# Kernel optimization log

Hardware: AMD Instinct MI355X
Metric: run time of the kernel (lower is better)

The kernel has to match this reference:

```python
import jax, jax.numpy as jnp
import numpy as np

B, C, H, W = 256, 512, 14, 14
HW = H * W
TAU = 0.03          # args.tau
EPS = 0.65          # args.epsilon
EPS2 = 0.40         # args.epsilon - args.epsilon_margin
T_LOGIT = 0.07      # args.logit_temperature
MAX_ITERS = 32      # static unrolled bound for the data-dependent while-loop
PD_EPS = 1e-6       # torch.nn.PairwiseDistance default eps (added to the difference)


def setup_inputs() -> dict:
    key = jax.random.key(0)
    k1, k2 = jax.random.split(key)
    img = jax.random.normal(k1, (B, C, H, W), jnp.float32)
    img = img / (jnp.linalg.norm(img, axis=1, keepdims=True) + 1e-12)  # L2 over channels
    aud = jax.random.normal(k2, (B, C), jnp.float32)
    aud = aud / (jnp.linalg.norm(aud, axis=1, keepdims=True) + 1e-12)
    return {"img": img, "aud": aud}


def reference(img, aud):
    Bb, Cc, Hh, Ww = img.shape
    n_pix = Hh * Ww

    # PosLogits: [B,1,H,W]; Alllogits: [B,B,H,W]
    pos_logits = jnp.einsum('ncqa,nc->nqa', img, aud)[:, None]
    all_logits = jnp.einsum('ncqa,kc->nkqa', img, aud)

    # trimap negatives
    pos2 = jax.nn.sigmoid((pos_logits - EPS2) / TAU)
    neg = 1.0 - pos2                                        # [B,1,H,W]

    logit = img.reshape(Bb, Cc, -1) * pos_logits.reshape(Bb, 1, -1)   # [B,C,HW]
    positive0 = pos_logits.reshape(Bb, -1)                            # [B,HW]
    neg_val = (logit * neg.reshape(Bb, 1, -1)).mean(axis=2)           # [B,C]

    logit_t = logit.transpose(0, 2, 1)                                 # [B,HW,C]
    dist_to_zero = jnp.linalg.norm(logit_t - neg_val[:, None, :] + PD_EPS, axis=-1)  # [B,HW]

    def body(t, state):
        positive, already_pos, endpoint, obj = state
        idx = jnp.argmax(positive, axis=1)                             # [B] (detached in torch)
        sel = jnp.take_along_axis(logit, idx[:, None, None], axis=2)[:, :, 0]  # [B,C]
        obj = obj.at[t].set(sel * (~endpoint)[:, None].astype(sel.dtype))
        dist_to_logit = jnp.linalg.norm(logit_t - sel[:, None, :] + PD_EPS, axis=-1)  # [B,HW]
        pos = (dist_to_logit < dist_to_zero) & (~already_pos)
        already_pos = already_pos | pos
        positive = positive * (1.0 - pos.astype(positive.dtype))
        endpoint = endpoint | (pos.sum(axis=1) == 0) | (positive.max(axis=1) < 0.1)
        return (positive, already_pos, endpoint, obj)

    obj0 = jnp.zeros((MAX_ITERS, Bb, Cc), img.dtype)
    state0 = (positive0,
              jnp.zeros((Bb, n_pix), bool),
              jnp.zeros((Bb,), bool),
              obj0)
    _, _, _, object_arr = jax.lax.fori_loop(0, MAX_ITERS, body, state0)

    # lvs contrastive loss
    mask = 1.0 - 100.0 * jnp.eye(Bb, dtype=img.dtype)
    pos_m = jax.nn.sigmoid((pos_logits - EPS) / TAU)                   # [B,1,H,W]
    pos_all = jax.nn.sigmoid((all_logits - EPS) / TAU)                 # [B,B,H,W]
    sim1 = (pos_m * pos_logits).reshape(Bb, 1, -1).sum(-1) / pos_m.reshape(Bb, 1, -1).sum(-1)
    sim = (pos_all * all_logits).reshape(Bb, Bb, -1).sum(-1) / pos_all.reshape(Bb, Bb, -1).sum(-1) * mask
    sim2 = (neg * pos_logits).reshape(Bb, 1, -1).sum(-1) / neg.reshape(Bb, 1, -1).sum(-1)
    logits = jnp.concatenate((sim1, sim, sim2), axis=1) / T_LOGIT      # [B, B+2]
    loss = -jax.nn.log_softmax(logits, axis=1)[:, 0].mean()           # CE with target 0

    return loss, pos_logits[:, 0], object_arr
```

## Files before the change

### kernel.cpp

```cpp
#include <hip/hip_runtime.h>
#include <hip/hip_bf16.h>
#include <math.h>

#define NB 256
#define NC 512
#define NP 196
#define NIT 32
#define PROWS 208
#define LSTR 72
#define SFSTR 211

typedef __attribute__((ext_vector_type(8))) short bf16x8;
typedef __attribute__((ext_vector_type(4))) float f32x4;

__device__ __forceinline__ float sigf(float z){ return 1.0f/(1.0f+expf(-z)); }

__device__ __forceinline__ unsigned short f2bf(float x){
  return __bfloat16_as_ushort(__float2bfloat16(x));
}
__device__ __forceinline__ float bf2f(unsigned short h){
  union{float f; unsigned u;} v; v.u = ((unsigned)h)<<16; return v.f;
}
__device__ __forceinline__ double dshfl_xor(double v, int m){
  int lo = __shfl_xor(__double2loint(v), m);
  int hi = __shfl_xor(__double2hiint(v), m);
  return __hiloint2double(hi, lo);
}

__global__ __launch_bounds__(256) void aud2bf_kernel(const float* __restrict__ aud, unsigned short* __restrict__ aud_bf)
{
  int i = blockIdx.x*256 + threadIdx.x;
  aud_bf[i] = f2bf(aud[i]);
}


__global__ __launch_bounds__(512) void convert4_kernel(
    const float* __restrict__ img, const float* __restrict__ aud,
    unsigned short* __restrict__ hiT, unsigned short* __restrict__ loT,
    double* __restrict__ ppl, double* __restrict__ pcs)
{
  const int bid = blockIdx.x;
  const int b = bid & 255, part = bid >> 8;
  const int tid = threadIdx.x;
  const float* imgb = img + (size_t)b*NC*NP + (size_t)part*64*NP;
  __shared__ float sf[64*SFSTR];
  __shared__ float s_aud[64];
  if (tid < 64) s_aud[tid] = aud[b*NC + part*64 + tid];

  for (int j=tid; j<64*49; j+=512){
    int p4 = j % 49, c = j / 49;
    float4 v = *(const float4*)&imgb[(size_t)c*NP + p4*4];
    sf[c*SFSTR + p4*4+0]=v.x; sf[c*SFSTR + p4*4+1]=v.y;
    sf[c*SFSTR + p4*4+2]=v.z; sf[c*SFSTR + p4*4+3]=v.w;
  }
  __syncthreads();

  unsigned short* hp = hiT + (size_t)(b*8+part)*PROWS*64;
  unsigned short* lp = loT + (size_t)(b*8+part)*PROWS*64;
  for (int j=tid; j<PROWS*8; j+=512){
    int p = j>>3, o = j&7;
    unsigned hw[4], lw[4];
    double dot=0.0, sm=0.0;
    #pragma unroll
    for (int k2=0;k2<4;++k2){
      int c = o*8 + 2*k2;
      float x0 = (p<NP) ? sf[c*SFSTR + p]     : 0.f;
      float x1 = (p<NP) ? sf[(c+1)*SFSTR + p] : 0.f;
      unsigned short h0=f2bf(x0), h1=f2bf(x1);
      unsigned short l0=f2bf(x0-bf2f(h0)), l1=f2bf(x1-bf2f(h1));
      hw[k2] = (unsigned)h0 | ((unsigned)h1<<16);
      lw[k2] = (unsigned)l0 | ((unsigned)l1<<16);
      dot += (double)x0*(double)s_aud[c] + (double)x1*(double)s_aud[c+1];
      sm  += (double)x0 + (double)x1;
    }
    if (p < NP){
      *(uint4*)&hp[p*64 + o*8] = *(uint4*)hw;
      *(uint4*)&lp[p*64 + o*8] = *(uint4*)lw;
    }
    dot += dshfl_xor(dot,1); dot += dshfl_xor(dot,2); dot += dshfl_xor(dot,4);
    sm  += dshfl_xor(sm,1);  sm  += dshfl_xor(sm,2);  sm  += dshfl_xor(sm,4);
    if (o==0 && p<NP){
      ppl[(size_t)(b*8+part)*NP + p] = dot;
      pcs[(size_t)(b*8+part)*NP + p] = sm;
    }
  }
}

__global__ __launch_bounds__(256) void prep3_kernel(
    const double* __restrict__ ppl, const double* __restrict__ pcs,
    float* __restrict__ pl, float* __restrict__ cs,
    float* __restrict__ sim1, float* __restrict__ sim2, float* __restrict__ out_pl)
{
  const int b = blockIdx.x, tid = threadIdx.x;
  __shared__ double s_redd[256];
  float plv=0.f;
  if (tid < NP){
    double a=0.0, s=0.0;
    #pragma unroll
    for (int part=0; part<8; ++part){
      a += ppl[(size_t)(b*8+part)*NP + tid];
      s += pcs[(size_t)(b*8+part)*NP + tid];
    }
    plv=(float)a;
    float csv=(float)s;
    pl[b*NP+tid]=plv; cs[b*NP+tid]=csv; out_pl[b*NP+tid]=plv;
  }
  float pmw = (tid<NP)? sigf((plv-0.65f)/0.03f) : 0.f;
  float negw= (tid<NP)? 1.0f - sigf((plv-0.40f)/0.03f) : 0.f;
  double r[4];
  r[0]=(tid<NP)?(double)pmw*(double)plv:0.0;
  r[1]=(tid<NP)?(double)pmw:0.0;
  r[2]=(tid<NP)?(double)negw*(double)plv:0.0;
  r[3]=(tid<NP)?(double)negw:0.0;
  double res[4];
  for (int i=0;i<4;++i){
    __syncthreads();
    s_redd[tid]=r[i];
    __syncthreads();
    for (int s=128;s>0;s>>=1){ if (tid<s) s_redd[tid]+=s_redd[tid+s]; __syncthreads(); }
    res[i]=s_redd[0];
  }
  if (tid==0){
    sim1[b]=(float)(res[0]/res[1]);
    sim2[b]=(float)(res[2]/res[3]);
  }
}

__global__ __launch_bounds__(512) void gram2_kernel(
    const unsigned short* __restrict__ hiT, const unsigned short* __restrict__ loT,
    float* __restrict__ G)
{
  const int bid = blockIdx.x;
  const int b = bid & 255, h = bid >> 8;
  const int cbase = 7*h, ncl = 7 - h;
  const int tid = threadIdx.x, lane = tid & 63, w = tid >> 6;
  const int nr = (w<5)?2:1;
  const unsigned short* hb = hiT + (size_t)b*8*PROWS*64;
  const unsigned short* lb = loT + (size_t)b*8*PROWS*64;
  float* Gb = G + (size_t)b*NP*NP;
  __shared__ short smh[PROWS*LSTR];
  __shared__ short sml[PROWS*LSTR];

  f32x4 acc[2][7];
  #pragma unroll
  for (int i=0;i<2;++i)
    #pragma unroll
    for (int j=0;j<7;++j) acc[i][j]=(f32x4){0,0,0,0};

  for (int sl=0; sl<8; ++sl){
    __syncthreads();
    for (int j=tid; j<PROWS*8; j+=512){
      int p = j>>3, o = j&7;
      size_t src = ((size_t)sl*PROWS + p)*64 + o*8;
      *(uint4*)&smh[p*LSTR + o*8] = *(const uint4*)(hb + src);
      *(uint4*)&sml[p*LSTR + o*8] = *(const uint4*)(lb + src);
    }
    __syncthreads();
    #pragma unroll
    for (int kk=0; kk<2; ++kk){
      bf16x8 Ah[2], Al[2];
      #pragma unroll
      for (int i=0;i<2;++i){
        if (i<nr){
          int r = (w + 8*i)*16 + (lane&15);
          Ah[i] = *(const bf16x8*)&smh[r*LSTR + kk*32 + (lane>>4)*8];
          Al[i] = *(const bf16x8*)&sml[r*LSTR + kk*32 + (lane>>4)*8];
        }
      }
      #pragma unroll
      for (int j=0;j<7;++j){
        if (j<ncl){
          int r = (cbase+j)*16 + (lane&15);
          bf16x8 Bh = *(const bf16x8*)&smh[r*LSTR + kk*32 + (lane>>4)*8];
          bf16x8 Bl = *(const bf16x8*)&sml[r*LSTR + kk*32 + (lane>>4)*8];
          #pragma unroll
          for (int i=0;i<2;++i){
            if (i<nr){
              acc[i][j] = __builtin_amdgcn_mfma_f32_16x16x32_bf16(Ah[i], Bh, acc[i][j], 0,0,0);
              acc[i][j] = __builtin_amdgcn_mfma_f32_16x16x32_bf16(Ah[i], Bl, acc[i][j], 0,0,0);
              acc[i][j] = __builtin_amdgcn_mfma_f32_16x16x32_bf16(Al[i], Bh, acc[i][j], 0,0,0);
            }
          }
        }
      }
    }
  }

  const int r0 = (lane>>4)*4, colL = lane & 15;
  #pragma unroll
  for (int i=0;i<2;++i){
    #pragma unroll
    for (int j=0;j<7;++j){
      if (i<nr && j<ncl){
        int row = (w+8*i)*16 + r0;
        int col = (cbase+j)*16 + colL;
        if (col < NP){
          #pragma unroll
          for (int jj=0;jj<4;++jj){
            if (row+jj < NP) Gb[(size_t)(row+jj)*NP + col] = acc[i][j][jj];
          }
        }
      }
    }
  }
}

__global__ __launch_bounds__(512) void simgemm2_kernel(
    const unsigned short* __restrict__ hiT, const unsigned short* __restrict__ aud_bf,
    float* __restrict__ sumWA, float* __restrict__ sumW)
{
  const int bid = blockIdx.x;
  const int b = bid & 255, h = bid >> 8;
  const int tid = threadIdx.x, lane = tid & 63, w = tid >> 6;
  const int wr = w >> 2, wc = w & 3;
  const int pbase = (wr==0)?0:7, npt = 7-wr;
  const unsigned short* hb = hiT + (size_t)b*8*PROWS*64;
  __shared__ short smh[PROWS*LSTR];
  __shared__ short sma[128*LSTR];
  __shared__ float sred[2][2][4][2][16];

  f32x4 acc[7][2];
  #pragma unroll
  for (int i=0;i<7;++i)
    #pragma unroll
    for (int n=0;n<2;++n) acc[i][n]=(f32x4){0,0,0,0};

  for (int sl=0; sl<8; ++sl){
    __syncthreads();
    for (int j=tid; j<PROWS*8; j+=512){
      int p = j>>3, o = j&7;
      *(uint4*)&smh[p*LSTR + o*8] = *(const uint4*)(hb + ((size_t)sl*PROWS + p)*64 + o*8);
    }
    for (int j=tid; j<128*8; j+=512){
      int n = j>>3, o = j&7;
      *(uint4*)&sma[n*LSTR + o*8] = *(const uint4*)(aud_bf + (size_t)(h*128+n)*NC + sl*64 + o*8);
    }
    __syncthreads();
    #pragma unroll
    for (int kk=0; kk<2; ++kk){
      bf16x8 Ah[7];
      #pragma unroll
      for (int i=0;i<7;++i){
        if (i<npt){
          int r = (pbase+i)*16 + (lane&15);
          Ah[i] = *(const bf16x8*)&smh[r*LSTR + kk*32 + (lane>>4)*8];
        }
      }
      #pragma unroll
      for (int n=0;n<2;++n){
        int r = (wc*2+n)*16 + (lane&15);
        bf16x8 Bn = *(const bf16x8*)&sma[r*LSTR + kk*32 + (lane>>4)*8];
        #pragma unroll
        for (int i=0;i<7;++i)
          if (i<npt)
            acc[i][n] = __builtin_amdgcn_mfma_f32_16x16x32_bf16(Ah[i], Bn, acc[i][n], 0,0,0);
      }
    }
  }

  float swa[2]={0,0}, sw[2]={0,0};
  #pragma unroll
  for (int n=0;n<2;++n){
    #pragma unroll
    for (int i=0;i<7;++i){
      if (i<npt){
        int rowbase = (pbase+i)*16 + (lane>>4)*4;
        #pragma unroll
        for (int jj=0;jj<4;++jj){
          if (rowbase+jj < NP){
            float v = acc[i][n][jj];
            float wgt = sigf((v-0.65f)/0.03f);
            swa[n] += wgt*v; sw[n] += wgt;
          }
        }
      }
    }
  }
  #pragma unroll
  for (int n=0;n<2;++n){
    swa[n] += __shfl_xor(swa[n],16); swa[n] += __shfl_xor(swa[n],32);
    sw[n]  += __shfl_xor(sw[n],16);  sw[n]  += __shfl_xor(sw[n],32);
  }
  if (lane < 16){
    #pragma unroll
    for (int n=0;n<2;++n){
      sred[0][wr][wc][n][lane] = swa[n];
      sred[1][wr][wc][n][lane] = sw[n];
    }
  }
  __syncthreads();
  if (tid < 128){
    int wc2 = tid>>5, n2 = (tid>>4)&1, col = tid&15;
    float a = sred[0][0][wc2][n2][col] + sred[0][1][wc2][n2][col];
    float s = sred[1][0][wc2][n2][col] + sred[1][1][wc2][n2][col];
    int kcol = h*128 + (wc2*2+n2)*16 + col;
    sumWA[(size_t)b*NB + kcol] = a;
    sumW [(size_t)b*NB + kcol] = s;
  }
}

__global__ __launch_bounds__(1024) void loop4_kernel(
    const float* __restrict__ pl, const float* __restrict__ cs,
    const float* __restrict__ G, int* __restrict__ qseq, int* __restrict__ zf)
{
  const int b = blockIdx.x, tid = threadIdx.x, lane = tid & 63, w = tid >> 6;
  const float* Gb = G + (size_t)b*NP*NP;
  __shared__ float sG[NP*NP];
  __shared__ float s_pl[NP], s_wl[NP], s_csL[NP], s_gd[NP];
  __shared__ double gwd[NP];
  __shared__ double s_wred[16];
  __shared__ double s_bc;

  #pragma unroll
  for (int k=0;k<10;++k){
    int j = k*1024 + tid;
    if (j < NP*NP/4) ((float4*)sG)[j] = ((const float4*)Gb)[j];
  }
  float negw_t = 0.f;
  if (tid < NP){
    float plv = pl[b*NP+tid];
    float csv = cs[b*NP+tid];
    s_pl[tid] = plv;
    s_csL[tid] = plv*csv;
    negw_t = 1.0f - sigf((plv-0.40f)/0.03f);
    s_wl[tid] = plv*negw_t;
    s_gd[tid] = Gb[(size_t)tid*NP + tid];
  }
  __syncthreads();

  {
    int p = tid >> 2, qg = tid & 3;
    double a = 0.0;
    if (p < NP){
      for (int q=qg*49; q<qg*49+49; ++q) a += (double)sG[q*NP + p] * (double)s_wl[q];
    }
    a += dshfl_xor(a,1); a += dshfl_xor(a,2);
    if (qg==0 && p<NP) gwd[p] = a;
  }
  __syncthreads();

  double r = (tid<NP) ? (double)s_wl[tid]*gwd[tid] : 0.0;
  #pragma unroll
  for (int m=1;m<64;m<<=1) r += dshfl_xor(r,m);
  if (lane==0) s_wred[w] = r;
  __syncthreads();
  if (tid==0){ double t=0.0; for (int i=0;i<16;++i) t += s_wred[i]; s_bc = t; }
  __syncthreads();
  const double S2 = s_bc;
  __syncthreads();

  r = (tid<NP) ? (double)negw_t*(double)s_csL[tid] : 0.0;
  #pragma unroll
  for (int m=1;m<64;m<<=1) r += dshfl_xor(r,m);
  if (lane==0) s_wred[w] = r;
  __syncthreads();
  if (tid==0){ double t=0.0; for (int i=0;i<16;++i) t += s_wred[i]; s_bc = t; }
  __syncthreads();
  const double Swl = s_bc;
  __syncthreads();

  if (tid < NP){
    const double e = (double)1e-6f;
    double pld = (double)s_pl[tid];
    double d0sq = pld*pld*(double)s_gd[tid]
                - (2.0/196.0)*pld*gwd[tid]
                + S2/(196.0*196.0)
                + 2.0*e*((double)s_csL[tid] - Swl/196.0)
                + 512.0*e*e;
    if (d0sq < 0.0) d0sq = 0.0;
    gwd[tid] = d0sq;
  }
  __syncthreads();

  if (w != 0) return;

  float plv[4], csL[4], gdd[4], posv[4];
  double d0sq[4];
  bool alr[4];
  #pragma unroll
  for (int s=0;s<4;++s){
    int p = lane + 64*s;
    bool valid = p < NP;
    plv[s]  = valid ? s_pl[p]  : 0.f;
    csL[s]  = valid ? s_csL[p] : 0.f;
    gdd[s]  = valid ? s_gd[p]  : 0.f;
    d0sq[s] = valid ? gwd[p]   : 0.0;
    posv[s] = valid ? plv[s]   : -INFINITY;
    alr[s] = false;
  }
  bool endp = false;

  for (int t=0;t<NIT;++t){
    float v = posv[0]; int ix = lane;
    #pragma unroll
    for (int s=1;s<4;++s){
      if (posv[s] > v){ v = posv[s]; ix = lane + 64*s; }
    }
    #pragma unroll
    for (int m=1;m<64;m<<=1){
      float vv = __shfl_xor(v, m);
      int   ii = __shfl_xor(ix, m);
      if (vv>v || (vv==v && ii<ix)){ v=vv; ix=ii; }
    }
    const int q = ix;
    const float plq  = s_pl[q];
    const float gqq  = s_gd[q];
    const float csLq = s_csL[q];
    if (lane==0){ qseq[b*NIT+t] = q; zf[b*NIT+t] = endp ? 1 : 0; }

    int cnt = 0;
    #pragma unroll
    for (int s=0;s<4;++s){
      int p = lane + 64*s;
      if (p<NP && !alr[s]){
        float Gpq = sG[q*NP + p];
        double plp=(double)plv[s], dq=(double)plq;
        const double e=(double)1e-6f;
        double d2 = plp*plp*(double)gdd[s]
                  - 2.0*plp*dq*(double)Gpq
                  + dq*dq*(double)gqq
                  + 2.0*e*((double)csL[s]-(double)csLq)
                  + 512.0*e*e;
        if (d2<0.0) d2=0.0;
        if (d2 < d0sq[s]){ alr[s]=true; posv[s]=posv[s]*0.0f; cnt++; }
      }
    }
    float mx = fmaxf(fmaxf(posv[0],posv[1]),fmaxf(posv[2],posv[3]));
    #pragma unroll
    for (int m=1;m<64;m<<=1){
      cnt += __shfl_xor(cnt, m);
      mx = fmaxf(mx, __shfl_xor(mx, m));
    }
    if (cnt==0 || mx<0.1f) endp=true;
  }
}

__global__ __launch_bounds__(64) void objw_kernel(
    const unsigned short* __restrict__ hiT, const unsigned short* __restrict__ loT,
    const float* __restrict__ pl, const int* __restrict__ qseq, const int* __restrict__ zf,
    float* __restrict__ obj)
{
  const int bid = blockIdx.x;
  const int b = bid >> 5, t = bid & 31;
  const int lane = threadIdx.x;
  float* op = obj + ((size_t)t*NB + b)*NC;
  const int z = zf[b*NIT + t];
  if (z){
    float4 zv = {0.f,0.f,0.f,0.f};
    *(float4*)&op[lane*8]   = zv;
    *(float4*)&op[lane*8+4] = zv;
    return;
  }
  const int q = qseq[b*NIT + t];
  const float plq = pl[b*NP + q];
  const int part = lane >> 3, off = lane & 7;
  size_t src = ((size_t)(b*8+part)*PROWS + q)*64 + off*8;
  uint4 hv = *(const uint4*)(hiT + src);
  uint4 lv = *(const uint4*)(loT + src);
  const unsigned* hw = (const unsigned*)&hv;
  const unsigned* lw = (const unsigned*)&lv;
  float o8[8];
  #pragma unroll
  for (int k2=0;k2<4;++k2){
    float x0 = bf2f((unsigned short)(hw[k2]&0xffff)) + bf2f((unsigned short)(lw[k2]&0xffff));
    float x1 = bf2f((unsigned short)(hw[k2]>>16))    + bf2f((unsigned short)(lw[k2]>>16));
    o8[2*k2]   = x0*plq;
    o8[2*k2+1] = x1*plq;
  }
  *(float4*)&op[lane*8]   = *(float4*)&o8[0];
  *(float4*)&op[lane*8+4] = *(float4*)&o8[4];
}

__global__ __launch_bounds__(256) void finalize_b(
    const float* __restrict__ sim1, const float* __restrict__ sim2,
    const float* __restrict__ sumWA, const float* __restrict__ sumW,
    float* __restrict__ lossb)
{
  const int b = blockIdx.x, k = threadIdx.x;
  __shared__ float s_red[256];
  __shared__ double s_redd[256];
  const float T = 0.07f;
  float s = sumWA[(size_t)b*NB+k]/sumW[(size_t)b*NB+k];
  if (k==b) s *= -99.0f;
  const float lk = s/T;
  const float l0 = sim1[b]/T, ll = sim2[b]/T;
  s_red[k]=lk; __syncthreads();
  for (int st=128;st>0;st>>=1){ if(k<st) s_red[k]=fmaxf(s_red[k],s_red[k+st]); __syncthreads(); }
  const float m = fmaxf(s_red[0], fmaxf(l0,ll));
  __syncthreads();
  double e = (double)expf(lk-m);
  if (k==0) e += (double)expf(l0-m)+(double)expf(ll-m);
  s_redd[k]=e; __syncthreads();
  for (int st=128;st>0;st>>=1){ if(k<st) s_redd[k]+=s_redd[k+st]; __syncthreads(); }
  if (k==0) lossb[b] = -(float)((double)(l0-m) - log(s_redd[0]));
}

__global__ __launch_bounds__(256) void finalize_sum(const float* __restrict__ lossb, float* __restrict__ out_loss)
{
  const int tid = threadIdx.x;
  __shared__ double sr[256];
  sr[tid]=(double)lossb[tid]; __syncthreads();
  for (int st=128;st>0;st>>=1){ if(tid<st) sr[tid]+=sr[tid+st]; __syncthreads(); }
  if (tid==0) out_loss[0]=(float)(sr[0]/256.0);
}

extern "C" void kernel_launch(void* const* d_in, const int* in_sizes, int n_in,
                              void* d_out, int out_size, void* d_ws, size_t ws_size,
                              hipStream_t stream)
{
  const float* img = (const float*)d_in[0];
  const float* aud = (const float*)d_in[1];
  float* out = (float*)d_out;
  float* ws  = (float*)d_ws;

  float* pl    = ws;
  float* cs    = pl    + NB*NP;
  float* sim1  = cs    + NB*NP;
  float* sim2  = sim1  + NB;
  float* sumWA = sim2  + NB;
  float* sumW  = sumWA + NB*NB;
  unsigned short* aud_bf = (unsigned short*)(sumW + NB*NB);
  float* G     = (float*)(aud_bf + NB*NC);
  unsigned short* hiT = (unsigned short*)(G + (size_t)NB*NP*NP);
  unsigned short* loT = hiT + (size_t)NB*8*PROWS*64;
  int* qseq    = (int*)(loT + (size_t)NB*8*PROWS*64);
  int* zf      = qseq + NB*NIT;
  float* lossb = (float*)(zf + NB*NIT);

  double* ppl = (double*)G;
  double* pcs = ppl + (size_t)NB*8*NP;

  float* out_loss = out;
  float* out_pl   = out + 1;
  float* out_obj  = out + 1 + NB*NP;

  hipLaunchKernelGGL(aud2bf_kernel,   dim3(NB*NC/256), dim3(256),  0, stream, aud, aud_bf);
  hipLaunchKernelGGL(convert4_kernel, dim3(NB*8),      dim3(512),  0, stream, img, aud, hiT, loT, ppl, pcs);
  hipLaunchKernelGGL(prep3_kernel,    dim3(NB),        dim3(256),  0, stream, ppl, pcs, pl, cs, sim1, sim2, out_pl);
  hipLaunchKernelGGL(gram2_kernel,    dim3(NB*2),      dim3(512),  0, stream, hiT, loT, G);
  hipLaunchKernelGGL(loop4_kernel,    dim3(NB),        dim3(1024), 0, stream, pl, cs, G, qseq, zf);
  hipLaunchKernelGGL(simgemm2_kernel, dim3(NB*2),      dim3(512),  0, stream, hiT, aud_bf, sumWA, sumW);
  hipLaunchKernelGGL(objw_kernel,     dim3(NB*NIT),    dim3(64),   0, stream, hiT, loT, pl, qseq, zf, out_obj);
  hipLaunchKernelGGL(finalize_b,      dim3(NB),        dim3(256),  0, stream, sim1, sim2, sumWA, sumW, lossb);
  hipLaunchKernelGGL(finalize_sum,    dim3(1),         dim3(256),  0, stream, lossb, out_loss);
}
```

Measured before the change: 200.2 us.

## Fuse gram and sim GEMMs, fold aud conversion and obj writeback into neighbours

```diff
diff --git a/kernel.cpp b/kernel.cpp
--- a/kernel.cpp
+++ b/kernel.cpp
@@ -27,16 +27,11 @@
   return __hiloint2double(hi, lo);
 }
 
-__global__ __launch_bounds__(256) void aud2bf_kernel(const float* __restrict__ aud, unsigned short* __restrict__ aud_bf)
-{
-  int i = blockIdx.x*256 + threadIdx.x;
-  aud_bf[i] = f2bf(aud[i]);
-}
-
 
 __global__ __launch_bounds__(512) void convert4_kernel(
     const float* __restrict__ img, const float* __restrict__ aud,
     unsigned short* __restrict__ hiT, unsigned short* __restrict__ loT,
+    unsigned short* __restrict__ aud_bf,
     double* __restrict__ ppl, double* __restrict__ pcs)
 {
   const int bid = blockIdx.x;
@@ -45,6 +40,7 @@
   const float* imgb = img + (size_t)b*NC*NP + (size_t)part*64*NP;
   __shared__ float sf[64*SFSTR];
   __shared__ float s_aud[64];
+  if (part == 0) aud_bf[b*NC + tid] = f2bf(aud[b*NC + tid]);
   if (tid < 64) s_aud[tid] = aud[b*NC + part*64 + tid];
 
   for (int j=tid; j<64*49; j+=512){
@@ -126,182 +122,180 @@
   }
 }
 
-__global__ __launch_bounds__(512) void gram2_kernel(
+__global__ __launch_bounds__(512) void gramsim_kernel(
     const unsigned short* __restrict__ hiT, const unsigned short* __restrict__ loT,
-    float* __restrict__ G)
+    const unsigned short* __restrict__ aud_bf,
+    float* __restrict__ G, float* __restrict__ sumWA, float* __restrict__ sumW)
 {
   const int bid = blockIdx.x;
-  const int b = bid & 255, h = bid >> 8;
-  const int cbase = 7*h, ncl = 7 - h;
+  const int xcd = bid & 7, k = bid >> 3;
+  const int b = xcd + 8*(k>>2), role = k & 3;
   const int tid = threadIdx.x, lane = tid & 63, w = tid >> 6;
-  const int nr = (w<5)?2:1;
   const unsigned short* hb = hiT + (size_t)b*8*PROWS*64;
   const unsigned short* lb = loT + (size_t)b*8*PROWS*64;
-  float* Gb = G + (size_t)b*NP*NP;
-  __shared__ short smh[PROWS*LSTR];
-  __shared__ short sml[PROWS*LSTR];
-
-  f32x4 acc[2][7];
-  #pragma unroll
-  for (int i=0;i<2;++i)
-    #pragma unroll
-    for (int j=0;j<7;++j) acc[i][j]=(f32x4){0,0,0,0};
-
-  for (int sl=0; sl<8; ++sl){
-    __syncthreads();
-    for (int j=tid; j<PROWS*8; j+=512){
-      int p = j>>3, o = j&7;
-      size_t src = ((size_t)sl*PROWS + p)*64 + o*8;
-      *(uint4*)&smh[p*LSTR + o*8] = *(const uint4*)(hb + src);
-      *(uint4*)&sml[p*LSTR + o*8] = *(const uint4*)(lb + src);
-    }
-    __syncthreads();
-    #pragma unroll
-    for (int kk=0; kk<2; ++kk){
-      bf16x8 Ah[2], Al[2];
-      #pragma unroll
-      for (int i=0;i<2;++i){
-        if (i<nr){
-          int r = (w + 8*i)*16 + (lane&15);
-          Ah[i] = *(const bf16x8*)&smh[r*LSTR + kk*32 + (lane>>4)*8];
-          Al[i] = *(const bf16x8*)&sml[r*LSTR + kk*32 + (lane>>4)*8];
-        }
-      }
-      #pragma unroll
-      for (int j=0;j<7;++j){
-        if (j<ncl){
-          int r = (cbase+j)*16 + (lane&15);
-          bf16x8 Bh = *(const bf16x8*)&smh[r*LSTR + kk*32 + (lane>>4)*8];
-          bf16x8 Bl = *(const bf16x8*)&sml[r*LSTR + kk*32 + (lane>>4)*8];
-          #pragma unroll
-          for (int i=0;i<2;++i){
-            if (i<nr){
-              acc[i][j] = __builtin_amdgcn_mfma_f32_16x16x32_bf16(Ah[i], Bh, acc[i][j], 0,0,0);
-              acc[i][j] = __builtin_amdgcn_mfma_f32_16x16x32_bf16(Ah[i], Bl, acc[i][j], 0,0,0);
-              acc[i][j] = __builtin_amdgcn_mfma_f32_16x16x32_bf16(Al[i], Bh, acc[i][j], 0,0,0);
+  __shared__ short smA[PROWS*LSTR];
+  __shared__ short smB[PROWS*LSTR];
+  __shared__ float sred[2][2][4][2][16];
+
+  if (role < 2){
+    const int h = role;
+    const int cbase = 7*h, ncl = 7 - h;
+    const int nr = (w<5)?2:1;
+    float* Gb = G + (size_t)b*NP*NP;
+
+    f32x4 acc[2][7];
+    #pragma unroll
+    for (int i=0;i<2;++i)
+      #pragma unroll
+      for (int j=0;j<7;++j) acc[i][j]=(f32x4){0,0,0,0};
+
+    for (int sl=0; sl<8; ++sl){
+      __syncthreads();
+      for (int j=tid; j<PROWS*8; j+=512){
+        int p = j>>3, o = j&7;
+        size_t src = ((size_t)sl*PROWS + p)*64 + o*8;
+        *(uint4*)&smA[p*LSTR + o*8] = *(const uint4*)(hb + src);
+        *(uint4*)&smB[p*LSTR + o*8] = *(const uint4*)(lb + src);
+      }
+      __syncthreads();
+      #pragma unroll
+      for (int kk=0; kk<2; ++kk){
+        bf16x8 Ah[2], Al[2];
+        #pragma unroll
+        for (int i=0;i<2;++i){
+          if (i<nr){
+            int r = (w + 8*i)*16 + (lane&15);
+            Ah[i] = *(const bf16x8*)&smA[r*LSTR + kk*32 + (lane>>4)*8];
+            Al[i] = *(const bf16x8*)&smB[r*LSTR + kk*32 + (lane>>4)*8];
+          }
+        }
+        #pragma unroll
+        for (int j=0;j<7;++j){
+          if (j<ncl){
+            int r = (cbase+j)*16 + (lane&15);
+            bf16x8 Bh = *(const bf16x8*)&smA[r*LSTR + kk*32 + (lane>>4)*8];
+            bf16x8 Bl = *(const bf16x8*)&smB[r*LSTR + kk*32 + (lane>>4)*8];
+            #pragma unroll
+            for (int i=0;i<2;++i){
+              if (i<nr){
+                acc[i][j] = __builtin_amdgcn_mfma_f32_16x16x32_bf16(Ah[i], Bh, acc[i][j], 0,0,0);
+                acc[i][j] = __builtin_amdgcn_mfma_f32_16x16x32_bf16(Ah[i], Bl, acc[i][j], 0,0,0);
+                acc[i][j] = __builtin_amdgcn_mfma_f32_16x16x32_bf16(Al[i], Bh, acc[i][j], 0,0,0);
+              }
             }
           }
         }
       }
     }
-  }
-
-  const int r0 = (lane>>4)*4, colL = lane & 15;
-  #pragma unroll
-  for (int i=0;i<2;++i){
-    #pragma unroll
-    for (int j=0;j<7;++j){
-      if (i<nr && j<ncl){
-        int row = (w+8*i)*16 + r0;
-        int col = (cbase+j)*16 + colL;
-        if (col < NP){
+
+    const int r0 = (lane>>4)*4, colL = lane & 15;
+    #pragma unroll
+    for (int i=0;i<2;++i){
+      #pragma unroll
+      for (int j=0;j<7;++j){
+        if (i<nr && j<ncl){
+          int row = (w+8*i)*16 + r0;
+          int col = (cbase+j)*16 + colL;
+          if (col < NP){
+            #pragma unroll
+            for (int jj=0;jj<4;++jj){
+              if (row+jj < NP) Gb[(size_t)(row+jj)*NP + col] = acc[i][j][jj];
+            }
+          }
+        }
+      }
+    }
+  } else {
+    const int h = role - 2;
+    const int wr = w >> 2, wc = w & 3;
+    const int pbase = (wr==0)?0:7, npt = 7-wr;
+
+    f32x4 acc[7][2];
+    #pragma unroll
+    for (int i=0;i<7;++i)
+      #pragma unroll
+      for (int n=0;n<2;++n) acc[i][n]=(f32x4){0,0,0,0};
+
+    for (int sl=0; sl<8; ++sl){
+      __syncthreads();
+      for (int j=tid; j<PROWS*8; j+=512){
+        int p = j>>3, o = j&7;
+        *(uint4*)&smA[p*LSTR + o*8] = *(const uint4*)(hb + ((size_t)sl*PROWS + p)*64 + o*8);
+      }
+      for (int j=tid; j<128*8; j+=512){
+        int n = j>>3, o = j&7;
+        *(uint4*)&smB[n*LSTR + o*8] = *(const uint4*)(aud_bf + (size_t)(h*128+n)*NC + sl*64 + o*8);
+      }
+      __syncthreads();
+      #pragma unroll
+      for (int kk=0; kk<2; ++kk){
+        bf16x8 Ah[7];
+        #pragma unroll
+        for (int i=0;i<7;++i){
+          if (i<npt){
+            int r = (pbase+i)*16 + (lane&15);
+            Ah[i] = *(const bf16x8*)&smA[r*LSTR + kk*32 + (lane>>4)*8];
+          }
+        }
+        #pragma unroll
+        for (int n=0;n<2;++n){
+          int r = (wc*2+n)*16 + (lane&15);
+          bf16x8 Bn = *(const bf16x8*)&smB[r*LSTR + kk*32 + (lane>>4)*8];
+          #pragma unroll
+          for (int i=0;i<7;++i)
+            if (i<npt)
+              acc[i][n] = __builtin_amdgcn_mfma_f32_16x16x32_bf16(Ah[i], Bn, acc[i][n], 0,0,0);
+        }
+      }
+    }
+
+    float swa[2]={0,0}, sw[2]={0,0};
+    #pragma unroll
+    for (int n=0;n<2;++n){
+      #pragma unroll
+      for (int i=0;i<7;++i){
+        if (i<npt){
+          int rowbase = (pbase+i)*16 + (lane>>4)*4;
           #pragma unroll
           for (int jj=0;jj<4;++jj){
-            if (row+jj < NP) Gb[(size_t)(row+jj)*NP + col] = acc[i][j][jj];
+            if (rowbase+jj < NP){
+              float v = acc[i][n][jj];
+              float wgt = sigf((v-0.65f)/0.03f);
+              swa[n] += wgt*v; sw[n] += wgt;
+            }
           }
         }
       }
     }
-  }
-}
-
-__global__ __launch_bounds__(512) void simgemm2_kernel(
-    const unsigned short* __restrict__ hiT, const unsigned short* __restrict__ aud_bf,
-    float* __restrict__ sumWA, float* __restrict__ sumW)
-{
-  const int bid = blockIdx.x;
-  const int b = bid & 255, h = bid >> 8;
-  const int tid = threadIdx.x, lane = tid & 63, w = tid >> 6;
-  const int wr = w >> 2, wc = w & 3;
-  const int pbase = (wr==0)?0:7, npt = 7-wr;
-  const unsigned short* hb = hiT + (size_t)b*8*PROWS*64;
-  __shared__ short smh[PROWS*LSTR];
-  __shared__ short sma[128*LSTR];
-  __shared__ float sred[2][2][4][2][16];
-
-  f32x4 acc[7][2];
-  #pragma unroll
-  for (int i=0;i<7;++i)
-    #pragma unroll
-    for (int n=0;n<2;++n) acc[i][n]=(f32x4){0,0,0,0};
-
-  for (int sl=0; sl<8; ++sl){
+    #pragma unroll
+    for (int n=0;n<2;++n){
+      swa[n] += __shfl_xor(swa[n],16); swa[n] += __shfl_xor(swa[n],32);
+      sw[n]  += __shfl_xor(sw[n],16);  sw[n]  += __shfl_xor(sw[n],32);
+    }
+    if (lane < 16){
+      #pragma unroll
+      for (int n=0;n<2;++n){
+        sred[0][wr][wc][n][lane] = swa[n];
+        sred[1][wr][wc][n][lane] = sw[n];
+      }
+    }
     __syncthreads();
-    for (int j=tid; j<PROWS*8; j+=512){
-      int p = j>>3, o = j&7;
-      *(uint4*)&smh[p*LSTR + o*8] = *(const uint4*)(hb + ((size_t)sl*PROWS + p)*64 + o*8);
-    }
-    for (int j=tid; j<128*8; j+=512){
-      int n = j>>3, o = j&7;
-      *(uint4*)&sma[n*LSTR + o*8] = *(const uint4*)(aud_bf + (size_t)(h*128+n)*NC + sl*64 + o*8);
-    }
-    __syncthreads();
-    #pragma unroll
-    for (int kk=0; kk<2; ++kk){
-      bf16x8 Ah[7];
-      #pragma unroll
-      for (int i=0;i<7;++i){
-        if (i<npt){
-          int r = (pbase+i)*16 + (lane&15);
-          Ah[i] = *(const bf16x8*)&smh[r*LSTR + kk*32 + (lane>>4)*8];
-        }
-      }
-      #pragma unroll
-      for (int n=0;n<2;++n){
-        int r = (wc*2+n)*16 + (lane&15);
-        bf16x8 Bn = *(const bf16x8*)&sma[r*LSTR + kk*32 + (lane>>4)*8];
-        #pragma unroll
-        for (int i=0;i<7;++i)
-          if (i<npt)
-            acc[i][n] = __builtin_amdgcn_mfma_f32_16x16x32_bf16(Ah[i], Bn, acc[i][n], 0,0,0);
-      }
-    }
-  }
-
-  float swa[2]={0,0}, sw[2]={0,0};
-  #pragma unroll
-  for (int n=0;n<2;++n){
-    #pragma unroll
-    for (int i=0;i<7;++i){
-      if (i<npt){
-        int rowbase = (pbase+i)*16 + (lane>>4)*4;
-        #pragma unroll
-        for (int jj=0;jj<4;++jj){
-          if (rowbase+jj < NP){
-            float v = acc[i][n][jj];
-            float wgt = sigf((v-0.65f)/0.03f);
-            swa[n] += wgt*v; sw[n] += wgt;
-          }
-        }
-      }
-    }
-  }
-  #pragma unroll
-  for (int n=0;n<2;++n){
-    swa[n] += __shfl_xor(swa[n],16); swa[n] += __shfl_xor(swa[n],32);
-    sw[n]  += __shfl_xor(sw[n],16);  sw[n]  += __shfl_xor(sw[n],32);
-  }
-  if (lane < 16){
-    #pragma unroll
-    for (int n=0;n<2;++n){
-      sred[0][wr][wc][n][lane] = swa[n];
-      sred[1][wr][wc][n][lane] = sw[n];
-    }
-  }
-  __syncthreads();
-  if (tid < 128){
-    int wc2 = tid>>5, n2 = (tid>>4)&1, col = tid&15;
-    float a = sred[0][0][wc2][n2][col] + sred[0][1][wc2][n2][col];
-    float s = sred[1][0][wc2][n2][col] + sred[1][1][wc2][n2][col];
-    int kcol = h*128 + (wc2*2+n2)*16 + col;
-    sumWA[(size_t)b*NB + kcol] = a;
-    sumW [(size_t)b*NB + kcol] = s;
-  }
-}
-
-__global__ __launch_bounds__(1024) void loop4_kernel(
+    if (tid < 128){
+      int wc2 = tid>>5, n2 = (tid>>4)&1, col = tid&15;
+      float a = sred[0][0][wc2][n2][col] + sred[0][1][wc2][n2][col];
+      float s = sred[1][0][wc2][n2][col] + sred[1][1][wc2][n2][col];
+      int kcol = h*128 + (wc2*2+n2)*16 + col;
+      sumWA[(size_t)b*NB + kcol] = a;
+      sumW [(size_t)b*NB + kcol] = s;
+    }
+  }
+}
+
+__global__ __launch_bounds__(1024) void loop5_kernel(
     const float* __restrict__ pl, const float* __restrict__ cs,
-    const float* __restrict__ G, int* __restrict__ qseq, int* __restrict__ zf)
+    const float* __restrict__ G,
+    const unsigned short* __restrict__ hiT, const unsigned short* __restrict__ loT,
+    float* __restrict__ obj)
 {
   const int b = blockIdx.x, tid = threadIdx.x, lane = tid & 63, w = tid >> 6;
   const float* Gb = G + (size_t)b*NP*NP;
@@ -310,6 +304,7 @@
   __shared__ double gwd[NP];
   __shared__ double s_wred[16];
   __shared__ double s_bc;
+  __shared__ int s_q[NIT]; __shared__ int s_z[NIT];
 
   #pragma unroll
   for (int k=0;k<10;++k){
@@ -372,103 +367,96 @@
   }
   __syncthreads();
 
-  if (w != 0) return;
-
-  float plv[4], csL[4], gdd[4], posv[4];
-  double d0sq[4];
-  bool alr[4];
-  #pragma unroll
-  for (int s=0;s<4;++s){
-    int p = lane + 64*s;
-    bool valid = p < NP;
-    plv[s]  = valid ? s_pl[p]  : 0.f;
-    csL[s]  = valid ? s_csL[p] : 0.f;
-    gdd[s]  = valid ? s_gd[p]  : 0.f;
-    d0sq[s] = valid ? gwd[p]   : 0.0;
-    posv[s] = valid ? plv[s]   : -INFINITY;
-    alr[s] = false;
-  }
-  bool endp = false;
-
-  for (int t=0;t<NIT;++t){
-    float v = posv[0]; int ix = lane;
-    #pragma unroll
-    for (int s=1;s<4;++s){
-      if (posv[s] > v){ v = posv[s]; ix = lane + 64*s; }
-    }
-    #pragma unroll
-    for (int m=1;m<64;m<<=1){
-      float vv = __shfl_xor(v, m);
-      int   ii = __shfl_xor(ix, m);
-      if (vv>v || (vv==v && ii<ix)){ v=vv; ix=ii; }
-    }
-    const int q = ix;
-    const float plq  = s_pl[q];
-    const float gqq  = s_gd[q];
-    const float csLq = s_csL[q];
-    if (lane==0){ qseq[b*NIT+t] = q; zf[b*NIT+t] = endp ? 1 : 0; }
-
-    int cnt = 0;
+  if (w == 0){
+    float plv[4], csL[4], gdd[4], posv[4];
+    double d0sq[4];
+    bool alr[4];
     #pragma unroll
     for (int s=0;s<4;++s){
       int p = lane + 64*s;
-      if (p<NP && !alr[s]){
-        float Gpq = sG[q*NP + p];
-        double plp=(double)plv[s], dq=(double)plq;
-        const double e=(double)1e-6f;
-        double d2 = plp*plp*(double)gdd[s]
-                  - 2.0*plp*dq*(double)Gpq
-                  + dq*dq*(double)gqq
-                  + 2.0*e*((double)csL[s]-(double)csLq)
-                  + 512.0*e*e;
-        if (d2<0.0) d2=0.0;
-        if (d2 < d0sq[s]){ alr[s]=true; posv[s]=posv[s]*0.0f; cnt++; }
-      }
-    }
-    float mx = fmaxf(fmaxf(posv[0],posv[1]),fmaxf(posv[2],posv[3]));
-    #pragma unroll
-    for (int m=1;m<64;m<<=1){
-      cnt += __shfl_xor(cnt, m);
-      mx = fmaxf(mx, __shfl_xor(mx, m));
-    }
-    if (cnt==0 || mx<0.1f) endp=true;
-  }
-}
-
-__global__ __launch_bounds__(64) void objw_kernel(
-    const unsigned short* __restrict__ hiT, const unsigned short* __restrict__ loT,
-    const float* __restrict__ pl, const int* __restrict__ qseq, const int* __restrict__ zf,
-    float* __restrict__ obj)
-{
-  const int bid = blockIdx.x;
-  const int b = bid >> 5, t = bid & 31;
-  const int lane = threadIdx.x;
-  float* op = obj + ((size_t)t*NB + b)*NC;
-  const int z = zf[b*NIT + t];
-  if (z){
-    float4 zv = {0.f,0.f,0.f,0.f};
-    *(float4*)&op[lane*8]   = zv;
-    *(float4*)&op[lane*8+4] = zv;
-    return;
-  }
-  const int q = qseq[b*NIT + t];
-  const float plq = pl[b*NP + q];
-  const int part = lane >> 3, off = lane & 7;
-  size_t src = ((size_t)(b*8+part)*PROWS + q)*64 + off*8;
-  uint4 hv = *(const uint4*)(hiT + src);
-  uint4 lv = *(const uint4*)(loT + src);
-  const unsigned* hw = (const unsigned*)&hv;
-  const unsigned* lw = (const unsigned*)&lv;
-  float o8[8];
-  #pragma unroll
-  for (int k2=0;k2<4;++k2){
-    float x0 = bf2f((unsigned short)(hw[k2]&0xffff)) + bf2f((unsigned short)(lw[k2]&0xffff));
-    float x1 = bf2f((unsigned short)(hw[k2]>>16))    + bf2f((unsigned short)(lw[k2]>>16));
-    o8[2*k2]   = x0*plq;
-    o8[2*k2+1] = x1*plq;
-  }
-  *(float4*)&op[lane*8]   = *(float4*)&o8[0];
-  *(float4*)&op[lane*8+4] = *(float4*)&o8[4];
+      bool valid = p < NP;
+      plv[s]  = valid ? s_pl[p]  : 0.f;
+      csL[s]  = valid ? s_csL[p] : 0.f;
+      gdd[s]  = valid ? s_gd[p]  : 0.f;
+      d0sq[s] = valid ? gwd[p]   : 0.0;
+      posv[s] = valid ? plv[s]   : -INFINITY;
+      alr[s] = false;
+    }
+    bool endp = false;
+
+    for (int t=0;t<NIT;++t){
+      float v = posv[0]; int ix = lane;
+      #pragma unroll
+      for (int s=1;s<4;++s){
+        if (posv[s] > v){ v = posv[s]; ix = lane + 64*s; }
+      }
+      #pragma unroll
+      for (int m=1;m<64;m<<=1){
+        float vv = __shfl_xor(v, m);
+        int   ii = __shfl_xor(ix, m);
+        if (vv>v || (vv==v && ii<ix)){ v=vv; ix=ii; }
+      }
+      const int q = ix;
+      const float plq  = s_pl[q];
+      const float gqq  = s_gd[q];
+      const float csLq = s_csL[q];
+      if (lane==0){ s_q[t] = q; s_z[t] = endp ? 1 : 0; }
+
+      int cnt = 0;
+      #pragma unroll
+      for (int s=0;s<4;++s){
+        int p = lane + 64*s;
+        if (p<NP && !alr[s]){
+          float Gpq = sG[q*NP + p];
+          double plp=(double)plv[s], dq=(double)plq;
+          const double e=(double)1e-6f;
+          double d2 = plp*plp*(double)gdd[s]
+                    - 2.0*plp*dq*(double)Gpq
+                    + dq*dq*(double)gqq
+                    + 2.0*e*((double)csL[s]-(double)csLq)
+                    + 512.0*e*e;
+          if (d2<0.0) d2=0.0;
+          if (d2 < d0sq[s]){ alr[s]=true; posv[s]=posv[s]*0.0f; cnt++; }
+        }
+      }
+      float mx = fmaxf(fmaxf(posv[0],posv[1]),fmaxf(posv[2],posv[3]));
+      #pragma unroll
+      for (int m=1;m<64;m<<=1){
+        cnt += __shfl_xor(cnt, m);
+        mx = fmaxf(mx, __shfl_xor(mx, m));
+      }
+      if (cnt==0 || mx<0.1f) endp=true;
+    }
+  }
+  __syncthreads();
+
+  for (int j=tid; j<NIT*64; j+=1024){
+    int t = j >> 6, l8 = j & 63;
+    int part = l8 >> 3, off = l8 & 7;
+    float o8[8];
+    if (s_z[t]){
+      #pragma unroll
+      for (int e=0;e<8;++e) o8[e]=0.f;
+    } else {
+      int q = s_q[t];
+      float plq = s_pl[q];
+      size_t src = ((size_t)(b*8+part)*PROWS + q)*64 + off*8;
+      uint4 hv = *(const uint4*)(hiT + src);
+      uint4 lv = *(const uint4*)(loT + src);
+      const unsigned* hw = (const unsigned*)&hv;
+      const unsigned* lw = (const unsigned*)&lv;
+      #pragma unroll
+      for (int k2=0;k2<4;++k2){
+        float x0 = bf2f((unsigned short)(hw[k2]&0xffff)) + bf2f((unsigned short)(lw[k2]&0xffff));
+        float x1 = bf2f((unsigned short)(hw[k2]>>16))    + bf2f((unsigned short)(lw[k2]>>16));
+        o8[2*k2]   = x0*plq;
+        o8[2*k2+1] = x1*plq;
+      }
+    }
+    float* op = obj + ((size_t)t*NB + b)*NC + l8*8;
+    *(float4*)&op[0] = *(float4*)&o8[0];
+    *(float4*)&op[4] = *(float4*)&o8[4];
+  }
 }
 
 __global__ __launch_bounds__(256) void finalize_b(
@@ -523,9 +511,7 @@
   float* G     = (float*)(aud_bf + NB*NC);
   unsigned short* hiT = (unsigned short*)(G + (size_t)NB*NP*NP);
   unsigned short* loT = hiT + (size_t)NB*8*PROWS*64;
-  int* qseq    = (int*)(loT + (size_t)NB*8*PROWS*64);
-  int* zf      = qseq + NB*NIT;
-  float* lossb = (float*)(zf + NB*NIT);
+  float* lossb = (float*)(loT + (size_t)NB*8*PROWS*64);
 
   double* ppl = (double*)G;
   double* pcs = ppl + (size_t)NB*8*NP;
@@ -534,13 +520,10 @@
   float* out_pl   = out + 1;
   float* out_obj  = out + 1 + NB*NP;
 
-  hipLaunchKernelGGL(aud2bf_kernel,   dim3(NB*NC/256), dim3(256),  0, stream, aud, aud_bf);
-  hipLaunchKernelGGL(convert4_kernel, dim3(NB*8),      dim3(512),  0, stream, img, aud, hiT, loT, ppl, pcs);
-  hipLaunchKernelGGL(prep3_kernel,    dim3(NB),        dim3(256),  0, stream, ppl, pcs, pl, cs, sim1, sim2, out_pl);
-  hipLaunchKernelGGL(gram2_kernel,    dim3(NB*2),      dim3(512),  0, stream, hiT, loT, G);
-  hipLaunchKernelGGL(loop4_kernel,    dim3(NB),        dim3(1024), 0, stream, pl, cs, G, qseq, zf);
-  hipLaunchKernelGGL(simgemm2_kernel, dim3(NB*2),      dim3(512),  0, stream, hiT, aud_bf, sumWA, sumW);
-  hipLaunchKernelGGL(objw_kernel,     dim3(NB*NIT),    dim3(64),   0, stream, hiT, loT, pl, qseq, zf, out_obj);
-  hipLaunchKernelGGL(finalize_b,      dim3(NB),        dim3(256),  0, stream, sim1, sim2, sumWA, sumW, lossb);
-  hipLaunchKernelGGL(finalize_sum,    dim3(1),         dim3(256),  0, stream, lossb, out_loss);
-}
+  hipLaunchKernelGGL(convert4_kernel, dim3(NB*8),  dim3(512),  0, stream, img, aud, hiT, loT, aud_bf, ppl, pcs);
+  hipLaunchKernelGGL(prep3_kernel,    dim3(NB),    dim3(256),  0, stream, ppl, pcs, pl, cs, sim1, sim2, out_pl);
+  hipLaunchKernelGGL(gramsim_kernel,  dim3(NB*4),  dim3(512),  0, stream, hiT, loT, aud_bf, G, sumWA, sumW);
+  hipLaunchKernelGGL(loop5_kernel,    dim3(NB),    dim3(1024), 0, stream, pl, cs, G, hiT, loT, out_obj);
+  hipLaunchKernelGGL(finalize_b,      dim3(NB),    dim3(256),  0, stream, sim1, sim2, sumWA, sumW, lossb);
+  hipLaunchKernelGGL(finalize_sum,    dim3(1),     dim3(256),  0, stream, lossb, out_loss);
+}
```

Result: slower. 233.8 us (+16.8%).
